# Optimization experiments

Measured on AMD Instinct MI355X. Metric: run time of the kernel, lower is better.

Reference implementation:

```python
import jax, jax.numpy as jnp
import numpy as np

ALPHA = 0.2  # leaky_relu negative slope
NFEAT = 3    # node_feat_size for final tanh slice


def _init_linear(key, out_f, in_f):
    kw, kb = jax.random.split(key)
    scale = 1.0 / np.sqrt(in_f)
    w = jax.random.uniform(kw, (out_f, in_f), jnp.float32, -scale, scale)
    b = jax.random.uniform(kb, (out_f,), jnp.float32, -scale, scale)
    return w, b


def setup_inputs() -> dict:
    key = jax.random.key(0)
    ks = jax.random.split(key, 8)
    B, N, H = 64, 100, 32
    inp = {"x": jax.random.normal(ks[0], (B, N, H), jnp.float32)}
    # fe: [65 -> 96 -> 160 -> 192]; fn: [224 -> 256 -> 256 -> 32]
    fe_dims = [(96, 65), (160, 96), (192, 160)]
    fn_dims = [(256, 224), (256, 256), (32, 256)]
    for i, (o, f) in enumerate(fe_dims):
        w, b = _init_linear(ks[1 + i], o, f)
        inp[f"fe_w{i}"] = w
        inp[f"fe_b{i}"] = b
    for i, (o, f) in enumerate(fn_dims):
        w, b = _init_linear(ks[4 + i], o, f)
        inp[f"fn_w{i}"] = w
        inp[f"fn_b{i}"] = b
    return inp


def _forward(x, fe_params, fn_params):
    B, N, H = x.shape
    # --- getA: all-pairs edge features (pos_diffs) ---
    x1 = jnp.broadcast_to(x[:, :, None, :], (B, N, N, H))  # sender i
    x2 = jnp.broadcast_to(x[:, None, :, :], (B, N, N, H))  # receiver j
    dists = jnp.linalg.norm(x2[..., :2] - x1[..., :2] + 1e-12, axis=-1, keepdims=True)
    A = jnp.concatenate([x1, x2, dists], axis=-1)  # [B,N,N,2H+1]
    # --- edge MLP (all layers with leaky_relu) ---
    for w, b in fe_params:
        A = jax.nn.leaky_relu(jnp.einsum("bijf,of->bijo", A, w) + b, ALPHA)
    # sum-aggregate over neighbor axis j
    A = jnp.sum(A, axis=2)  # [B,N,fe_out]
    # --- node MLP (leaky_relu on all but last) ---
    h = jnp.concatenate([A, x], axis=-1)  # [B,N,fe_out+H]
    for w, b in fn_params[:-1]:
        h = jax.nn.leaky_relu(jnp.einsum("bnf,of->bno", h, w) + b, ALPHA)
    w, b = fn_params[-1]
    h = jnp.einsum("bnf,of->bno", h, w) + b  # [B,N,H]
    return jnp.tanh(h[..., :NFEAT])


def reference(x, fe_w0, fe_b0, fe_w1, fe_b1, fe_w2, fe_b2,
              fn_w0, fn_b0, fn_w1, fn_b1, fn_w2, fn_b2):
    fe_params = [(fe_w0, fe_b0), (fe_w1, fe_b1), (fe_w2, fe_b2)]
    fn_params = [(fn_w0, fn_b0), (fn_w1, fn_b1), (fn_w2, fn_b2)]
    return _forward(x, fe_params, fn_params)
```

## Files before the change

### kernel.cpp

```cpp
#include <hip/hip_runtime.h>
#include <math.h>

#define ALPHA 0.2f

typedef __attribute__((ext_vector_type(8))) short bf16x8;
typedef __attribute__((ext_vector_type(4))) float f32x4;

static __device__ __forceinline__ float lrelu(float v) {
    return fmaxf(v, ALPHA * v);
}
static __device__ __forceinline__ uint16_t f2b(float f) {
    union { float f; uint32_t u; } c; c.f = f;
    const uint32_t u = c.u + 0x7FFFu + ((c.u >> 16) & 1u);
    return (uint16_t)(u >> 16);
}
static __device__ __forceinline__ uint32_t cvt2(float lo, float hi) {
    uint32_t r;
    asm("v_cvt_pk_bf16_f32 %0, %1, %2" : "=v"(r) : "v"(lo), "v"(hi));
    return r;
}

__global__ __launch_bounds__(256) void precompute(
    const float* __restrict__ x, const float* __restrict__ w0,
    const float* __restrict__ b0, const float* __restrict__ w1,
    const float* __restrict__ w2, const float* __restrict__ f0,
    const float* __restrict__ f1,
    float* __restrict__ base0T, float* __restrict__ GT,
    float* __restrict__ xyt, float* __restrict__ wd0,
    uint16_t* __restrict__ wb1, uint16_t* __restrict__ wb2,
    uint16_t* __restrict__ wfn0, uint16_t* __restrict__ wfn1,
    float* __restrict__ hin)
{
    const int blk = blockIdx.x, t = threadIdx.x;
    if (blk >= 100) {
        const int t0 = (blk - 100) * 256 + t;
        for (int i = t0; i < 160 * 96;  i += 7168) wb1[i]  = f2b(w1[i]);
        for (int i = t0; i < 192 * 160; i += 7168) wb2[i]  = f2b(w2[i]);
        for (int i = t0; i < 256 * 224; i += 7168) wfn0[i] = f2b(f0[i]);
        for (int i = t0; i < 256 * 256; i += 7168) wfn1[i] = f2b(f1[i]);
        if (t0 < 96) wd0[t0] = w0[t0 * 65 + 64];
        return;
    }
    __shared__ float W0s[96 * 65];
    __shared__ float xs[64 * 32];
    const int r0 = blk * 64;
    for (int i = t; i < 96 * 65; i += 256) W0s[i] = w0[i];
    for (int i = t; i < 2048; i += 256) xs[i] = x[(size_t)r0 * 32 + i];
    __syncthreads();
    for (int it = 0; it < 48; ++it) {
        const int out = t + 256 * it;
        const int row = out / 192, oi = out - row * 192;
        const int o = (oi < 96) ? oi : oi - 96;
        const float* wr = W0s + o * 65 + ((oi < 96) ? 0 : 32);
        const float* xr = xs + row * 32;
        float a = (oi < 96) ? b0[o] : 0.0f;
#pragma unroll
        for (int k = 0; k < 32; ++k) a += wr[k] * xr[k];
        if (oi < 96) base0T[(size_t)(r0 + row) * 96 + o] = a;
        else         GT[(size_t)(r0 + row) * 96 + o] = a;
    }
    for (int i = t; i < 128; i += 256)
        xyt[(r0 + (i >> 1)) * 2 + (i & 1)] = xs[(i >> 1) * 32 + (i & 1)];
    for (int i = t; i < 2048; i += 256)
        hin[(size_t)(r0 + (i >> 5)) * 256 + 192 + (i & 31)] = xs[i];
}

__global__ __launch_bounds__(256, 3) void edge_kernel(
    const float* __restrict__ base0T, const float* __restrict__ GT,
    const float* __restrict__ xyt, const float* __restrict__ wd0,
    const float* __restrict__ b1f, const float* __restrict__ eb2,
    const uint16_t* __restrict__ wb1, const uint16_t* __restrict__ wb2,
    float* __restrict__ hin, float* __restrict__ PB)
{
    __shared__ __align__(16) uint16_t H1[64 * 104];
    __shared__ __align__(16) uint16_t H2l[64 * 168];

    const int bi = blockIdx.x >> 1, half = blockIdx.x & 1;
    const int b = bi / 100;
    const int MT = half ? 3 : 4;
    const int j0 = half * 64;
    const int t = threadIdx.x, lane = t & 63, wave = t >> 6;
    const int col = lane & 15, g = lane >> 4;

    {
        const int row = t >> 2, ch = t & 3;
        if (row < MT * 16) {
            const int jl = j0 + row;
            uint16_t* dst = H1 + row * 104 + ch * 24;
            if (jl < 100) {
                const int jg = b * 100 + jl;
                const float2 p  = *(const float2*)(xyt + 2 * jg);
                const float2 pi = *(const float2*)(xyt + 2 * bi);
                const float dx = p.x - pi.x + 1e-12f, dy = p.y - pi.y + 1e-12f;
                const float d = sqrtf(dx * dx + dy * dy);
                const float* gr = GT + (size_t)jg * 96 + ch * 24;
                const float* bb = base0T + (size_t)bi * 96 + ch * 24;
                const float* wv = wd0 + ch * 24;
                uint32_t pk[12];
#pragma unroll
                for (int q = 0; q < 6; ++q) {
                    const f32x4 gq = *(const f32x4*)(gr + q * 4);
                    const f32x4 bq = *(const f32x4*)(bb + q * 4);
                    const f32x4 wq = *(const f32x4*)(wv + q * 4);
                    float v[4];
#pragma unroll
                    for (int e = 0; e < 4; ++e)
                        v[e] = lrelu(gq[e] + bq[e] + wq[e] * d);
                    pk[2 * q]     = cvt2(v[0], v[1]);
                    pk[2 * q + 1] = cvt2(v[2], v[3]);
                }
#pragma unroll
                for (int q = 0; q < 3; ++q)
                    *(uint4*)(dst + q * 8) =
                        (uint4){pk[4 * q], pk[4 * q + 1], pk[4 * q + 2], pk[4 * q + 3]};
            } else {
                const uint4 z = {0u, 0u, 0u, 0u};
#pragma unroll
                for (int q = 0; q < 3; ++q) *(uint4*)(dst + q * 8) = z;
            }
        }
    }
    __syncthreads();

    {
        f32x4 acc[3][4];
#pragma unroll
        for (int s = 0; s < 3; ++s) {
            const int nt = wave + 4 * s;
            if (nt < 10) {
                const float bv = b1f[nt * 16 + col];
#pragma unroll
                for (int m = 0; m < 4; ++m) if (m < MT)
                    acc[s][m] = (f32x4){bv, bv, bv, bv};
            }
        }
        __builtin_amdgcn_s_setprio(1);
#pragma unroll
        for (int kt = 0; kt < 3; ++kt) {
            bf16x8 bfr[3];
#pragma unroll
            for (int s = 0; s < 3; ++s) {
                const int nt = wave + 4 * s;
                if (nt < 10)
                    bfr[s] = *(const bf16x8*)(wb1 + (size_t)(nt * 16 + col) * 96 + kt * 32 + 8 * g);
            }
#pragma unroll
            for (int m = 0; m < 4; ++m) if (m < MT) {
                const bf16x8 af = *(const bf16x8*)(H1 + (m * 16 + col) * 104 + kt * 32 + 8 * g);
#pragma unroll
                for (int s = 0; s < 3; ++s) {
                    const int nt = wave + 4 * s;
                    if (nt < 10)
                        acc[s][m] = __builtin_amdgcn_mfma_f32_16x16x32_bf16(af, bfr[s], acc[s][m], 0, 0, 0);
                }
            }
        }
        __builtin_amdgcn_s_setprio(0);
#pragma unroll
        for (int s = 0; s < 3; ++s) {
            const int nt = wave + 4 * s;
            if (nt < 10) {
#pragma unroll
                for (int m = 0; m < 4; ++m) if (m < MT) {
                    const uint32_t p01 = cvt2(lrelu(acc[s][m][0]), lrelu(acc[s][m][1]));
                    const uint32_t p23 = cvt2(lrelu(acc[s][m][2]), lrelu(acc[s][m][3]));
                    const int base = (m * 16 + 4 * g) * 168 + nt * 16 + col;
                    H2l[base]       = (uint16_t)p01;
                    H2l[base + 168] = (uint16_t)(p01 >> 16);
                    H2l[base + 336] = (uint16_t)p23;
                    H2l[base + 504] = (uint16_t)(p23 >> 16);
                }
            }
        }
    }
    __syncthreads();

    float ssum[3] = {0.f, 0.f, 0.f};
    {
        f32x4 acc[3][4];
#pragma unroll
        for (int s = 0; s < 3; ++s) {
            const float bv = eb2[(wave + 4 * s) * 16 + col];
#pragma unroll
            for (int m = 0; m < 4; ++m) if (m < MT)
                acc[s][m] = (f32x4){bv, bv, bv, bv};
        }
        __builtin_amdgcn_s_setprio(1);
#pragma unroll
        for (int kt = 0; kt < 5; ++kt) {
            bf16x8 bfr[3];
#pragma unroll
            for (int s = 0; s < 3; ++s)
                bfr[s] = *(const bf16x8*)(wb2 + (size_t)((wave + 4 * s) * 16 + col) * 160 + kt * 32 + 8 * g);
#pragma unroll
            for (int m = 0; m < 4; ++m) if (m < MT) {
                const bf16x8 af = *(const bf16x8*)(H2l + (m * 16 + col) * 168 + kt * 32 + 8 * g);
#pragma unroll
                for (int s = 0; s < 3; ++s)
                    acc[s][m] = __builtin_amdgcn_mfma_f32_16x16x32_bf16(af, bfr[s], acc[s][m], 0, 0, 0);
            }
        }
        __builtin_amdgcn_s_setprio(0);
#pragma unroll
        for (int s = 0; s < 3; ++s) {
#pragma unroll
            for (int m = 0; m < 4; ++m) if (m < MT) {
                const bool rowok = (MT == 4) || (m < 2) || (g == 0);
                if (rowok) {
#pragma unroll
                    for (int r = 0; r < 4; ++r) ssum[s] += lrelu(acc[s][m][r]);
                }
            }
        }
    }
    float* dst = (half == 0) ? (hin + (size_t)bi * 256) : (PB + (size_t)bi * 192);
#pragma unroll
    for (int s = 0; s < 3; ++s) {
        float v = ssum[s];
        v += __shfl_xor(v, 16);
        v += __shfl_xor(v, 32);
        if (lane < 16) dst[(wave + 4 * s) * 16 + col] = v;
    }
}

__global__ __launch_bounds__(256) void node_kernel(
    const float* __restrict__ hin, const float* __restrict__ PB,
    const uint16_t* __restrict__ wfn0, const float* __restrict__ fb0,
    const uint16_t* __restrict__ wfn1, const float* __restrict__ fb1,
    const float* __restrict__ fw2, const float* __restrict__ fb2,
    float* __restrict__ out)
{
    __shared__ __align__(16) uint16_t RA[16 * 264];
    __shared__ __align__(16) uint16_t RH[16 * 264];
    const int t = threadIdx.x, lane = t & 63, wave = t >> 6;
    const int col = lane & 15, g = lane >> 4;
    const int r0 = blockIdx.x * 16;

    for (int r = wave; r < 16; r += 4) {
        const float* src = hin + (size_t)(r0 + r) * 256;
        const float* pbr = PB + (size_t)(r0 + r) * 192;
        for (int c = lane; c < 224; c += 64) {
            float v = src[c];
            if (c < 192) v += pbr[c];
            RA[r * 232 + c] = f2b(v);
        }
    }
    __syncthreads();
    {
        f32x4 acc[4];
#pragma unroll
        for (int s = 0; s < 4; ++s) {
            const float bv = fb0[(wave + 4 * s) * 16 + col];
            acc[s] = (f32x4){bv, bv, bv, bv};
        }
#pragma unroll
        for (int kt = 0; kt < 7; ++kt) {
            const bf16x8 af = *(const bf16x8*)(RA + col * 232 + kt * 32 + 8 * g);
#pragma unroll
            for (int s = 0; s < 4; ++s) {
                const bf16x8 bfr = *(const bf16x8*)(
                    wfn0 + (size_t)((wave + 4 * s) * 16 + col) * 224 + kt * 32 + 8 * g);
                acc[s] = __builtin_amdgcn_mfma_f32_16x16x32_bf16(af, bfr, acc[s], 0, 0, 0);
            }
        }
#pragma unroll
        for (int s = 0; s < 4; ++s)
#pragma unroll
            for (int r = 0; r < 4; ++r)
                RH[(4 * g + r) * 264 + (wave + 4 * s) * 16 + col] = f2b(lrelu(acc[s][r]));
    }
    __syncthreads();
    {
        f32x4 acc[4];
#pragma unroll
        for (int s = 0; s < 4; ++s) {
            const float bv = fb1[(wave + 4 * s) * 16 + col];
            acc[s] = (f32x4){bv, bv, bv, bv};
        }
#pragma unroll
        for (int kt = 0; kt < 8; ++kt) {
            const bf16x8 af = *(const bf16x8*)(RH + col * 264 + kt * 32 + 8 * g);
#pragma unroll
            for (int s = 0; s < 4; ++s) {
                const bf16x8 bfr = *(const bf16x8*)(
                    wfn1 + (size_t)((wave + 4 * s) * 16 + col) * 256 + kt * 32 + 8 * g);
                acc[s] = __builtin_amdgcn_mfma_f32_16x16x32_bf16(af, bfr, acc[s], 0, 0, 0);
            }
        }
        __syncthreads();
#pragma unroll
        for (int s = 0; s < 4; ++s)
#pragma unroll
            for (int r = 0; r < 4; ++r)
                RA[(4 * g + r) * 264 + (wave + 4 * s) * 16 + col] = f2b(lrelu(acc[s][r]));
    }
    __syncthreads();
    const int row = t >> 4, u = t & 15;
    float h = 0.0f;
    if (u < 12) {
        const int o = u >> 2, ks = u & 3;
        const float* w = fw2 + o * 256 + ks * 64;
        const uint16_t* hr = RA + row * 264 + ks * 64;
        float a = 0.0f;
#pragma unroll 8
        for (int k = 0; k < 64; k += 4) {
            const ushort4 hv = *(const ushort4*)(hr + k);
            union { uint32_t u; float f; } c0, c1, c2, c3;
            c0.u = (uint32_t)hv.x << 16; c1.u = (uint32_t)hv.y << 16;
            c2.u = (uint32_t)hv.z << 16; c3.u = (uint32_t)hv.w << 16;
            a += w[k] * c0.f + w[k + 1] * c1.f + w[k + 2] * c2.f + w[k + 3] * c3.f;
        }
        h = a;
    }
    h += __shfl_xor(h, 1);
    h += __shfl_xor(h, 2);
    if (u < 12 && (u & 3) == 0)
        out[(size_t)(r0 + row) * 3 + (u >> 2)] = tanhf(h + fb2[u >> 2]);
}

extern "C" void kernel_launch(void* const* d_in, const int* in_sizes, int n_in,
                              void* d_out, int out_size, void* d_ws, size_t ws_size,
                              hipStream_t stream) {
    (void)in_sizes; (void)n_in; (void)out_size; (void)ws_size;
    const float* x     = (const float*)d_in[0];
    const float* fe_w0 = (const float*)d_in[1];
    const float* fe_b0 = (const float*)d_in[2];
    const float* fe_w1 = (const float*)d_in[3];
    const float* fe_b1 = (const float*)d_in[4];
    const float* fe_w2 = (const float*)d_in[5];
    const float* fe_b2 = (const float*)d_in[6];
    const float* fn_w0 = (const float*)d_in[7];
    const float* fn_b0 = (const float*)d_in[8];
    const float* fn_w1 = (const float*)d_in[9];
    const float* fn_b1 = (const float*)d_in[10];
    const float* fn_w2 = (const float*)d_in[11];
    const float* fn_b2 = (const float*)d_in[12];
    float* out = (float*)d_out;

    float* buf0   = (float*)d_ws;
    float* base0T = buf0 + (size_t)6400 * 256;
    float* GT     = base0T + 6400 * 96;
    float* xyt    = GT + 6400 * 96;
    float* wd0    = xyt + 12800;
    uint16_t* wb1  = (uint16_t*)(wd0 + 128);
    uint16_t* wb2  = wb1 + 160 * 96;
    uint16_t* wfn0 = wb2 + 192 * 160;
    uint16_t* wfn1 = wfn0 + 256 * 224;
    float* PB = (float*)(wfn1 + 256 * 256);

    precompute<<<128, 256, 0, stream>>>(x, fe_w0, fe_b0, fe_w1, fe_w2,
                                        fn_w0, fn_w1,
                                        base0T, GT, xyt, wd0,
                                        wb1, wb2, wfn0, wfn1, buf0);
    edge_kernel<<<12800, 256, 0, stream>>>(base0T, GT, xyt, wd0,
                                           fe_b1, fe_b2, wb1, wb2, buf0, PB);
    node_kernel<<<400, 256, 0, stream>>>(buf0, PB, wfn0, fn_b0, wfn1, fn_b1,
                                         fn_w2, fn_b2, out);
}
```

Baseline: 168.9 us.

## Build layer-1 A fragments in registers with a chunked G layout and remap waves to rows

The edge kernel drops the H1 shared-memory stage. Each lane now computes its layer-0 activation fragment straight into MFMA A registers, reading from a new chunk-of-8 interleaved G layout that precompute writes. Waves now own row tiles instead of column tiles, so every wave runs all the N tiles of both MLP layers, and the neighbour-sum reduction goes through a small shared partial-sum buffer. Precompute is regridded to 25 rows per block. This removes one LDS round trip and a barrier, but every wave now reads all the weight fragments from global memory, and the upper half-block computes padded rows that are wasted work.

New measurement: 338.1 us. +100.2%, slower.

```diff
diff --git a/kernel.cpp b/kernel.cpp
--- a/kernel.cpp
+++ b/kernel.cpp
@@ -25,15 +25,15 @@
     const float* __restrict__ b0, const float* __restrict__ w1,
     const float* __restrict__ w2, const float* __restrict__ f0,
     const float* __restrict__ f1,
-    float* __restrict__ base0T, float* __restrict__ GT,
+    float* __restrict__ base0T, float* __restrict__ Gp,
     float* __restrict__ xyt, float* __restrict__ wd0,
     uint16_t* __restrict__ wb1, uint16_t* __restrict__ wb2,
     uint16_t* __restrict__ wfn0, uint16_t* __restrict__ wfn1,
     float* __restrict__ hin)
 {
     const int blk = blockIdx.x, t = threadIdx.x;
-    if (blk >= 100) {
-        const int t0 = (blk - 100) * 256 + t;
+    if (blk >= 256) {
+        const int t0 = (blk - 256) * 256 + t;
         for (int i = t0; i < 160 * 96;  i += 7168) wb1[i]  = f2b(w1[i]);
         for (int i = t0; i < 192 * 160; i += 7168) wb2[i]  = f2b(w2[i]);
         for (int i = t0; i < 256 * 224; i += 7168) wfn0[i] = f2b(f0[i]);
@@ -42,184 +42,149 @@
         return;
     }
     __shared__ float W0s[96 * 65];
-    __shared__ float xs[64 * 32];
-    const int r0 = blk * 64;
+    __shared__ float xs[25 * 32];
+    const int r0 = blk * 25;
     for (int i = t; i < 96 * 65; i += 256) W0s[i] = w0[i];
-    for (int i = t; i < 2048; i += 256) xs[i] = x[(size_t)r0 * 32 + i];
-    __syncthreads();
-    for (int it = 0; it < 48; ++it) {
-        const int out = t + 256 * it;
-        const int row = out / 192, oi = out - row * 192;
-        const int o = (oi < 96) ? oi : oi - 96;
-        const float* wr = W0s + o * 65 + ((oi < 96) ? 0 : 32);
-        const float* xr = xs + row * 32;
-        float a = (oi < 96) ? b0[o] : 0.0f;
-#pragma unroll
-        for (int k = 0; k < 32; ++k) a += wr[k] * xr[k];
-        if (oi < 96) base0T[(size_t)(r0 + row) * 96 + o] = a;
-        else         GT[(size_t)(r0 + row) * 96 + o] = a;
-    }
-    for (int i = t; i < 128; i += 256)
+    for (int i = t; i < 800; i += 256) xs[i] = x[(size_t)r0 * 32 + i];
+    __syncthreads();
+    for (int it = 0; it < 19; ++it) {
+        const int q = t + 256 * it;
+        if (q < 4800) {
+            const int row = q / 192, oi = q - row * 192;
+            const int o = (oi < 96) ? oi : oi - 96;
+            const float* wr = W0s + o * 65 + ((oi < 96) ? 0 : 32);
+            const float* xr = xs + row * 32;
+            float a = (oi < 96) ? b0[o] : 0.0f;
+#pragma unroll
+            for (int k = 0; k < 32; ++k) a += wr[k] * xr[k];
+            if (oi < 96) base0T[(size_t)(r0 + row) * 96 + o] = a;
+            else         Gp[(size_t)(o >> 3) * 51200 + (size_t)(r0 + row) * 8 + (o & 7)] = a;
+        }
+    }
+    for (int i = t; i < 50; i += 256)
         xyt[(r0 + (i >> 1)) * 2 + (i & 1)] = xs[(i >> 1) * 32 + (i & 1)];
-    for (int i = t; i < 2048; i += 256)
+    for (int i = t; i < 800; i += 256)
         hin[(size_t)(r0 + (i >> 5)) * 256 + 192 + (i & 31)] = xs[i];
 }
 
 __global__ __launch_bounds__(256, 3) void edge_kernel(
-    const float* __restrict__ base0T, const float* __restrict__ GT,
+    const float* __restrict__ base0T, const float* __restrict__ Gp,
     const float* __restrict__ xyt, const float* __restrict__ wd0,
-    const float* __restrict__ b1f, const float* __restrict__ eb2,
+    const float* __restrict__ b1f, const float* __restrict__ b2f,
     const uint16_t* __restrict__ wb1, const uint16_t* __restrict__ wb2,
     float* __restrict__ hin, float* __restrict__ PB)
 {
-    __shared__ __align__(16) uint16_t H1[64 * 104];
     __shared__ __align__(16) uint16_t H2l[64 * 168];
-
-    const int bi = blockIdx.x >> 1, half = blockIdx.x & 1;
-    const int b = bi / 100;
-    const int MT = half ? 3 : 4;
-    const int j0 = half * 64;
-    const int t = threadIdx.x, lane = t & 63, wave = t >> 6;
+    __shared__ __align__(16) float part[4][192];
+
+    const int bi = blockIdx.x >> 1, half = blockIdx.x & 1, b = bi / 100;
+    const int t = threadIdx.x, lane = t & 63, m = t >> 6;
     const int col = lane & 15, g = lane >> 4;
 
-    {
-        const int row = t >> 2, ch = t & 3;
-        if (row < MT * 16) {
-            const int jl = j0 + row;
-            uint16_t* dst = H1 + row * 104 + ch * 24;
-            if (jl < 100) {
-                const int jg = b * 100 + jl;
-                const float2 p  = *(const float2*)(xyt + 2 * jg);
-                const float2 pi = *(const float2*)(xyt + 2 * bi);
-                const float dx = p.x - pi.x + 1e-12f, dy = p.y - pi.y + 1e-12f;
-                const float d = sqrtf(dx * dx + dy * dy);
-                const float* gr = GT + (size_t)jg * 96 + ch * 24;
-                const float* bb = base0T + (size_t)bi * 96 + ch * 24;
-                const float* wv = wd0 + ch * 24;
-                uint32_t pk[12];
-#pragma unroll
-                for (int q = 0; q < 6; ++q) {
-                    const f32x4 gq = *(const f32x4*)(gr + q * 4);
-                    const f32x4 bq = *(const f32x4*)(bb + q * 4);
-                    const f32x4 wq = *(const f32x4*)(wv + q * 4);
-                    float v[4];
-#pragma unroll
-                    for (int e = 0; e < 4; ++e)
-                        v[e] = lrelu(gq[e] + bq[e] + wq[e] * d);
-                    pk[2 * q]     = cvt2(v[0], v[1]);
-                    pk[2 * q + 1] = cvt2(v[2], v[3]);
-                }
-#pragma unroll
-                for (int q = 0; q < 3; ++q)
-                    *(uint4*)(dst + q * 8) =
-                        (uint4){pk[4 * q], pk[4 * q + 1], pk[4 * q + 2], pk[4 * q + 3]};
-            } else {
-                const uint4 z = {0u, 0u, 0u, 0u};
-#pragma unroll
-                for (int q = 0; q < 3; ++q) *(uint4*)(dst + q * 8) = z;
+    const int jloc = half * 64 + m * 16 + col;
+    const int jc = (jloc < 100) ? jloc : 99;
+    const int jg = b * 100 + jc;
+
+    const float2 pj = *(const float2*)(xyt + 2 * jg);
+    const float2 pi = *(const float2*)(xyt + 2 * bi);
+    const float dx = pj.x - pi.x + 1e-12f, dy = pj.y - pi.y + 1e-12f;
+    const float d = sqrtf(dx * dx + dy * dy);
+
+    bf16x8 af[3];
+#pragma unroll
+    for (int kt = 0; kt < 3; ++kt) {
+        const int ow = kt * 32 + 8 * g;
+        const float* gp = Gp + (size_t)(kt * 4 + g) * 51200 + (size_t)jg * 8;
+        const f32x4 g0 = *(const f32x4*)(gp);
+        const f32x4 g1 = *(const f32x4*)(gp + 4);
+        const f32x4 c0 = *(const f32x4*)(base0T + (size_t)bi * 96 + ow);
+        const f32x4 c1 = *(const f32x4*)(base0T + (size_t)bi * 96 + ow + 4);
+        const f32x4 w0v = *(const f32x4*)(wd0 + ow);
+        const f32x4 w1v = *(const f32x4*)(wd0 + ow + 4);
+        float v[8];
+#pragma unroll
+        for (int e = 0; e < 4; ++e) {
+            v[e]     = lrelu(g0[e] + c0[e] + w0v[e] * d);
+            v[4 + e] = lrelu(g1[e] + c1[e] + w1v[e] * d);
+        }
+        union { uint32_t u[4]; bf16x8 h; } cv;
+        cv.u[0] = cvt2(v[0], v[1]); cv.u[1] = cvt2(v[2], v[3]);
+        cv.u[2] = cvt2(v[4], v[5]); cv.u[3] = cvt2(v[6], v[7]);
+        af[kt] = cv.h;
+    }
+
+#pragma unroll
+    for (int p = 0; p < 2; ++p) {
+        f32x4 acc[5];
+#pragma unroll
+        for (int s = 0; s < 5; ++s) {
+            const float bv = b1f[(p * 5 + s) * 16 + col];
+            acc[s] = (f32x4){bv, bv, bv, bv};
+        }
+        __builtin_amdgcn_s_setprio(1);
+#pragma unroll
+        for (int kt = 0; kt < 3; ++kt) {
+#pragma unroll
+            for (int s = 0; s < 5; ++s) {
+                const bf16x8 bfr = *(const bf16x8*)(
+                    wb1 + (size_t)((p * 5 + s) * 16 + col) * 96 + kt * 32 + 8 * g);
+                acc[s] = __builtin_amdgcn_mfma_f32_16x16x32_bf16(af[kt], bfr, acc[s], 0, 0, 0);
             }
         }
-    }
-    __syncthreads();
-
-    {
-        f32x4 acc[3][4];
-#pragma unroll
-        for (int s = 0; s < 3; ++s) {
-            const int nt = wave + 4 * s;
-            if (nt < 10) {
-                const float bv = b1f[nt * 16 + col];
-#pragma unroll
-                for (int m = 0; m < 4; ++m) if (m < MT)
-                    acc[s][m] = (f32x4){bv, bv, bv, bv};
+        __builtin_amdgcn_s_setprio(0);
+#pragma unroll
+        for (int s = 0; s < 5; ++s) {
+            const uint32_t p01 = cvt2(lrelu(acc[s][0]), lrelu(acc[s][1]));
+            const uint32_t p23 = cvt2(lrelu(acc[s][2]), lrelu(acc[s][3]));
+            const int base = (m * 16 + 4 * g) * 168 + (p * 5 + s) * 16 + col;
+            H2l[base]       = (uint16_t)p01;
+            H2l[base + 168] = (uint16_t)(p01 >> 16);
+            H2l[base + 336] = (uint16_t)p23;
+            H2l[base + 504] = (uint16_t)(p23 >> 16);
+        }
+    }
+    __syncthreads();
+
+    const int rowbase = half * 64 + m * 16 + 4 * g;
+#pragma unroll
+    for (int p = 0; p < 2; ++p) {
+        f32x4 acc[6];
+#pragma unroll
+        for (int s = 0; s < 6; ++s) {
+            const float bv = b2f[(p * 6 + s) * 16 + col];
+            acc[s] = (f32x4){bv, bv, bv, bv};
+        }
+        bf16x8 a3[5];
+#pragma unroll
+        for (int kt = 0; kt < 5; ++kt)
+            a3[kt] = *(const bf16x8*)(H2l + (m * 16 + col) * 168 + kt * 32 + 8 * g);
+        __builtin_amdgcn_s_setprio(1);
+#pragma unroll
+        for (int kt = 0; kt < 5; ++kt) {
+#pragma unroll
+            for (int s = 0; s < 6; ++s) {
+                const bf16x8 bfr = *(const bf16x8*)(
+                    wb2 + (size_t)((p * 6 + s) * 16 + col) * 160 + kt * 32 + 8 * g);
+                acc[s] = __builtin_amdgcn_mfma_f32_16x16x32_bf16(a3[kt], bfr, acc[s], 0, 0, 0);
             }
         }
-        __builtin_amdgcn_s_setprio(1);
-#pragma unroll
-        for (int kt = 0; kt < 3; ++kt) {
-            bf16x8 bfr[3];
-#pragma unroll
-            for (int s = 0; s < 3; ++s) {
-                const int nt = wave + 4 * s;
-                if (nt < 10)
-                    bfr[s] = *(const bf16x8*)(wb1 + (size_t)(nt * 16 + col) * 96 + kt * 32 + 8 * g);
-            }
-#pragma unroll
-            for (int m = 0; m < 4; ++m) if (m < MT) {
-                const bf16x8 af = *(const bf16x8*)(H1 + (m * 16 + col) * 104 + kt * 32 + 8 * g);
-#pragma unroll
-                for (int s = 0; s < 3; ++s) {
-                    const int nt = wave + 4 * s;
-                    if (nt < 10)
-                        acc[s][m] = __builtin_amdgcn_mfma_f32_16x16x32_bf16(af, bfr[s], acc[s][m], 0, 0, 0);
-                }
-            }
-        }
         __builtin_amdgcn_s_setprio(0);
 #pragma unroll
-        for (int s = 0; s < 3; ++s) {
-            const int nt = wave + 4 * s;
-            if (nt < 10) {
-#pragma unroll
-                for (int m = 0; m < 4; ++m) if (m < MT) {
-                    const uint32_t p01 = cvt2(lrelu(acc[s][m][0]), lrelu(acc[s][m][1]));
-                    const uint32_t p23 = cvt2(lrelu(acc[s][m][2]), lrelu(acc[s][m][3]));
-                    const int base = (m * 16 + 4 * g) * 168 + nt * 16 + col;
-                    H2l[base]       = (uint16_t)p01;
-                    H2l[base + 168] = (uint16_t)(p01 >> 16);
-                    H2l[base + 336] = (uint16_t)p23;
-                    H2l[base + 504] = (uint16_t)(p23 >> 16);
-                }
-            }
-        }
-    }
-    __syncthreads();
-
-    float ssum[3] = {0.f, 0.f, 0.f};
-    {
-        f32x4 acc[3][4];
-#pragma unroll
-        for (int s = 0; s < 3; ++s) {
-            const float bv = eb2[(wave + 4 * s) * 16 + col];
-#pragma unroll
-            for (int m = 0; m < 4; ++m) if (m < MT)
-                acc[s][m] = (f32x4){bv, bv, bv, bv};
-        }
-        __builtin_amdgcn_s_setprio(1);
-#pragma unroll
-        for (int kt = 0; kt < 5; ++kt) {
-            bf16x8 bfr[3];
-#pragma unroll
-            for (int s = 0; s < 3; ++s)
-                bfr[s] = *(const bf16x8*)(wb2 + (size_t)((wave + 4 * s) * 16 + col) * 160 + kt * 32 + 8 * g);
-#pragma unroll
-            for (int m = 0; m < 4; ++m) if (m < MT) {
-                const bf16x8 af = *(const bf16x8*)(H2l + (m * 16 + col) * 168 + kt * 32 + 8 * g);
-#pragma unroll
-                for (int s = 0; s < 3; ++s)
-                    acc[s][m] = __builtin_amdgcn_mfma_f32_16x16x32_bf16(af, bfr[s], acc[s][m], 0, 0, 0);
-            }
-        }
-        __builtin_amdgcn_s_setprio(0);
-#pragma unroll
-        for (int s = 0; s < 3; ++s) {
-#pragma unroll
-            for (int m = 0; m < 4; ++m) if (m < MT) {
-                const bool rowok = (MT == 4) || (m < 2) || (g == 0);
-                if (rowok) {
-#pragma unroll
-                    for (int r = 0; r < 4; ++r) ssum[s] += lrelu(acc[s][m][r]);
-                }
-            }
-        }
-    }
-    float* dst = (half == 0) ? (hin + (size_t)bi * 256) : (PB + (size_t)bi * 192);
-#pragma unroll
-    for (int s = 0; s < 3; ++s) {
-        float v = ssum[s];
-        v += __shfl_xor(v, 16);
-        v += __shfl_xor(v, 32);
-        if (lane < 16) dst[(wave + 4 * s) * 16 + col] = v;
+        for (int s = 0; s < 6; ++s) {
+            float ps = 0.0f;
+#pragma unroll
+            for (int r = 0; r < 4; ++r)
+                if (rowbase + r < 100) ps += lrelu(acc[s][r]);
+            ps += __shfl_xor(ps, 16);
+            ps += __shfl_xor(ps, 32);
+            if (lane < 16) part[m][(p * 6 + s) * 16 + col] = ps;
+        }
+    }
+    __syncthreads();
+    if (t < 192) {
+        const float v = part[0][t] + part[1][t] + part[2][t] + part[3][t];
+        if (half == 0) hin[(size_t)bi * 256 + t] = v;
+        else           PB[(size_t)bi * 192 + t] = v;
     }
 }
 
@@ -255,12 +220,12 @@
         }
 #pragma unroll
         for (int kt = 0; kt < 7; ++kt) {
-            const bf16x8 af = *(const bf16x8*)(RA + col * 232 + kt * 32 + 8 * g);
+            const bf16x8 afr = *(const bf16x8*)(RA + col * 232 + kt * 32 + 8 * g);
 #pragma unroll
             for (int s = 0; s < 4; ++s) {
                 const bf16x8 bfr = *(const bf16x8*)(
                     wfn0 + (size_t)((wave + 4 * s) * 16 + col) * 224 + kt * 32 + 8 * g);
-                acc[s] = __builtin_amdgcn_mfma_f32_16x16x32_bf16(af, bfr, acc[s], 0, 0, 0);
+                acc[s] = __builtin_amdgcn_mfma_f32_16x16x32_bf16(afr, bfr, acc[s], 0, 0, 0);
             }
         }
 #pragma unroll
@@ -279,12 +244,12 @@
         }
 #pragma unroll
         for (int kt = 0; kt < 8; ++kt) {
-            const bf16x8 af = *(const bf16x8*)(RH + col * 264 + kt * 32 + 8 * g);
+            const bf16x8 afr = *(const bf16x8*)(RH + col * 264 + kt * 32 + 8 * g);
 #pragma unroll
             for (int s = 0; s < 4; ++s) {
                 const bf16x8 bfr = *(const bf16x8*)(
                     wfn1 + (size_t)((wave + 4 * s) * 16 + col) * 256 + kt * 32 + 8 * g);
-                acc[s] = __builtin_amdgcn_mfma_f32_16x16x32_bf16(af, bfr, acc[s], 0, 0, 0);
+                acc[s] = __builtin_amdgcn_mfma_f32_16x16x32_bf16(afr, bfr, acc[s], 0, 0, 0);
             }
         }
         __syncthreads();
@@ -339,8 +304,8 @@
 
     float* buf0   = (float*)d_ws;
     float* base0T = buf0 + (size_t)6400 * 256;
-    float* GT     = base0T + 6400 * 96;
-    float* xyt    = GT + 6400 * 96;
+    float* Gp     = base0T + 6400 * 96;
+    float* xyt    = Gp + 6400 * 96;
     float* wd0    = xyt + 12800;
     uint16_t* wb1  = (uint16_t*)(wd0 + 128);
     uint16_t* wb2  = wb1 + 160 * 96;
@@ -348,11 +313,11 @@
     uint16_t* wfn1 = wfn0 + 256 * 224;
     float* PB = (float*)(wfn1 + 256 * 256);
 
-    precompute<<<128, 256, 0, stream>>>(x, fe_w0, fe_b0, fe_w1, fe_w2,
+    precompute<<<284, 256, 0, stream>>>(x, fe_w0, fe_b0, fe_w1, fe_w2,
                                         fn_w0, fn_w1,
-                                        base0T, GT, xyt, wd0,
+                                        base0T, Gp, xyt, wd0,
                                         wb1, wb2, wfn0, wfn1, buf0);
-    edge_kernel<<<12800, 256, 0, stream>>>(base0T, GT, xyt, wd0,
+    edge_kernel<<<12800, 256, 0, stream>>>(base0T, Gp, xyt, wd0,
                                            fe_b1, fe_b2, wb1, wb2, buf0, PB);
     node_kernel<<<400, 256, 0, stream>>>(buf0, PB, wfn0, fn_b0, wfn1, fn_b1,
                                          fn_w2, fn_b2, out);
```
